# Performance work log

Hardware: AMD Instinct MI355X
Metric: run time of the kernel (lower is better)

## Reference

```python
import jax, jax.numpy as jnp
import numpy as np

B, T, D, H, NB = 4, 2048, 128, 4, 2
DK = D // H
LN_EPS = 1e-3  # keras LayerNormalization default epsilon


def _pos_encoding(maxlen, d):
    # faithful to TransformerNet.get_position_encoding (flat pos-major layout)
    pe = np.array([pos / np.power(10000, 2 * i / d) for pos in range(maxlen) for i in range(d)])
    pe[::2] = np.sin(pe[::2])
    pe[1::2] = np.cos(pe[1::2])
    return jnp.asarray(pe.reshape(maxlen, d), dtype=jnp.float32)


def _ln(x, g, b):
    mu = jnp.mean(x, axis=-1, keepdims=True)
    var = jnp.mean(jnp.square(x - mu), axis=-1, keepdims=True)
    return g * (x - mu) / jnp.sqrt(var + LN_EPS) + b


def setup_inputs() -> dict:
    key = jax.random.key(0)
    ks = jax.random.split(key, 14)
    s = 1.0 / np.sqrt(D)
    w = lambda k, shape: (jax.random.normal(k, shape, jnp.float32) * s)
    return {
        'inputs': jax.random.normal(ks[0], (B, T, D), jnp.float32),
        'Wq': w(ks[1], (NB, D, D)), 'bq': jnp.zeros((NB, D), jnp.float32),
        'Wk': w(ks[2], (NB, D, D)), 'bk': jnp.zeros((NB, D), jnp.float32),
        'Wv': w(ks[3], (NB, D, D)), 'bv': jnp.zeros((NB, D), jnp.float32),
        'Wo': w(ks[4], (NB, D, D)), 'bo': jnp.zeros((NB, D), jnp.float32),
        'W1': w(ks[5], (NB, D, D)), 'b1': jnp.zeros((NB, D), jnp.float32),
        'W2': w(ks[6], (NB, D, D)), 'b2': jnp.zeros((NB, D), jnp.float32),
        'ln_g': jnp.ones((2 * NB, D), jnp.float32),
        'ln_b': jnp.zeros((2 * NB, D), jnp.float32),
    }


def reference(inputs, Wq, bq, Wk, bk, Wv, bv, Wo, bo, W1, b1, W2, b2, ln_g, ln_b):
    h = inputs + _pos_encoding(T, D)[None]  # [B,T,D]
    scale = 1.0 / jnp.sqrt(jnp.float32(DK))
    for i in range(NB):
        # pre-attention LayerNorm
        h = _ln(h, ln_g[2 * i], ln_b[2 * i])
        q = (h @ Wq[i] + bq[i]).reshape(B, T, H, DK)
        k = (h @ Wk[i] + bk[i]).reshape(B, T, H, DK)
        v = (h @ Wv[i] + bv[i]).reshape(B, T, H, DK)
        scores = jnp.einsum('bqhd,bkhd->bhqk', q, k) * scale
        p = jax.nn.softmax(scores, axis=-1)
        # mask is None in TransformerNet.call, but the renormalize step remains
        attn = p / (jnp.sum(p, axis=-1, keepdims=True) + 1e-8)
        ctx = jnp.einsum('bhqk,bkhd->bqhd', attn, v).reshape(B, T, D)
        h = ctx @ Wo[i] + bo[i]  # no residual around attention (as in source)
        # pre-FFN LayerNorm
        h = _ln(h, ln_g[2 * i + 1], ln_b[2 * i + 1])
        # FeedForward with internal residual
        h = h + (jnp.maximum(h @ W1[i] + b1[i], 0.0) @ W2[i] + b2[i])
    # final norm reuses norm_layers[-1] == norm_layers[2*NB-1] (source quirk)
    return _ln(h, ln_g[-1], ln_b[-1])
```

## Files before the change

### kernel.cpp

```cpp
#include <hip/hip_runtime.h>
#include <hip/hip_bf16.h>

typedef __bf16 bf16x8 __attribute__((ext_vector_type(8)));
typedef __bf16 bf16x4 __attribute__((ext_vector_type(4)));
typedef float f32x4 __attribute__((ext_vector_type(4)));
typedef float f32x16 __attribute__((ext_vector_type(16)));
typedef unsigned int u32x4v __attribute__((ext_vector_type(4)));

#define D_ 128
#define T_ 2048
#define B_ 4
#define H_ 4
#define NB_ 2


__global__ __launch_bounds__(256) void prep_weights(
    const float* __restrict__ Wq, const float* __restrict__ Wk,
    const float* __restrict__ Wv, const float* __restrict__ Wo,
    const float* __restrict__ W1, const float* __restrict__ W2,
    __bf16* __restrict__ wp)
{
  int tid = blockIdx.x * 256 + threadIdx.x;
  int e    = tid & 7;
  int lane = (tid >> 3) & 63;
  int ks   = (tid >> 9) & 3;
  int nt   = (tid >> 11) & 7;
  int i    = (tid >> 14) & (NB_ - 1);
  int j    = tid >> 15;
  int k = ks * 32 + (lane >> 4) * 8 + e;
  int n = nt * 16 + (lane & 15);
  const float* srcs[6] = {Wq, Wk, Wv, Wo, W1, W2};
  wp[tid] = (__bf16)srcs[j][i * 16384 + k * 128 + n];
}

__global__ __launch_bounds__(256) void posadd(
    const float* __restrict__ x, __bf16* __restrict__ hp)
{
  int w = threadIdx.x >> 6, lane = threadIdx.x & 63;
  int row = blockIdx.x * 4 + w;
  int t = row & (T_ - 1);
  #pragma unroll
  for (int e = 0; e < 2; e++) {
    int c = lane * 2 + e;
    float arg = (float)t * exp2f(-0.20762050593045952f * (float)c);
    float pe = (c & 1) ? cosf(arg) : sinf(arg);
    float v = x[row * D_ + c] + pe;
    size_t idx = ((size_t)(row >> 4) * 4 + (c >> 5)) * 512 +
                 ((row & 15) + 16 * ((c >> 3) & 3)) * 8 + (c & 7);
    hp[idx] = (__bf16)v;
  }
}

__global__ __launch_bounds__(256) void lnqkv(
    const __bf16* __restrict__ hp, const __bf16* __restrict__ wpq,
    const __bf16* __restrict__ wpk, const __bf16* __restrict__ wpv,
    const float* __restrict__ bq, const float* __restrict__ bk,
    const float* __restrict__ bv, const float* __restrict__ g,
    const float* __restrict__ beta,
    __bf16* __restrict__ qp, __bf16* __restrict__ kp, __bf16* __restrict__ vp)
{
  int w = threadIdx.x >> 6, lane = threadIdx.x & 63;
  int m0 = blockIdx.x * 16;
  int lr = lane & 15, kg = lane >> 4;

  bf16x8 araw[4];
  #pragma unroll
  for (int ks = 0; ks < 4; ks++)
    araw[ks] = *(const bf16x8*)(hp + ((size_t)blockIdx.x * 4 + ks) * 512 + lane * 8);

  float s = 0.f, s2 = 0.f;
  #pragma unroll
  for (int ks = 0; ks < 4; ks++)
    #pragma unroll
    for (int e = 0; e < 8; e++) {
      float x = (float)araw[ks][e];
      s += x; s2 += x * x;
    }
  s += __shfl_xor(s, 16, 64);  s2 += __shfl_xor(s2, 16, 64);
  s += __shfl_xor(s, 32, 64);  s2 += __shfl_xor(s2, 32, 64);
  float mu = s * (1.f / D_);
  float var = s2 * (1.f / D_) - mu * mu;
  float rstd = rsqrtf(var + 1e-3f);

  bf16x8 af[4];
  #pragma unroll
  for (int ks = 0; ks < 4; ks++) {
    int c0 = ks * 32 + kg * 8;
    float4 g0 = *(const float4*)(g + c0), g1 = *(const float4*)(g + c0 + 4);
    float4 q0 = *(const float4*)(beta + c0), q1 = *(const float4*)(beta + c0 + 4);
    const float* gp[2] = {&g0.x, &g1.x};
    const float* bp[2] = {&q0.x, &q1.x};
    #pragma unroll
    for (int e = 0; e < 8; e++)
      af[ks][e] = (__bf16)(((float)araw[ks][e] - mu) * rstd * gp[e >> 2][e & 3] + bp[e >> 2][e & 3]);
  }

  #pragma unroll
  for (int i = 0; i < 2; i++) {
    int nt = w * 2 + i;
    const __bf16* wq = wpq + (size_t)(nt * 4) * 512 + lane * 8;
    const __bf16* wk = wpk + (size_t)(nt * 4) * 512 + lane * 8;
    const __bf16* wv = wpv + (size_t)(nt * 4) * 512 + lane * 8;
    f32x4 aq = {0, 0, 0, 0}, ak = {0, 0, 0, 0}, av = {0, 0, 0, 0};
    #pragma unroll
    for (int ks = 0; ks < 4; ks++) {
      aq = __builtin_amdgcn_mfma_f32_16x16x32_bf16(af[ks], *(const bf16x8*)(wq + ks * 512), aq, 0, 0, 0);
      ak = __builtin_amdgcn_mfma_f32_16x16x32_bf16(af[ks], *(const bf16x8*)(wk + ks * 512), ak, 0, 0, 0);
      av = __builtin_amdgcn_mfma_f32_16x16x32_bf16(af[ks], *(const bf16x8*)(wv + ks * 512), av, 0, 0, 0);
    }
    int col = nt * 16 + lr;
    float bqc = bq[col], bkc = bk[col], bvc = bv[col];
    int dk = i * 16 + lr;
    int hi8 = (lr >> 3) & 1;
    #pragma unroll
    for (int r = 0; r < 4; r++) {
      int row = m0 + kg * 4 + r;
      int bb = row >> 11, tt = row & (T_ - 1);
      size_t qidx = ((((size_t)(bb * 64 + (tt >> 5)) * 4 + w) * 2 + i) * 512) +
                    ((tt & 31) + 32 * hi8) * 8 + (lr & 7);
      qp[qidx] = (__bf16)(aq[r] + bqc);
      size_t kidx = ((((size_t)(bb * 4 + w) * 64 + (tt >> 5)) * 2 + i) * 512) +
                    ((tt & 31) + 32 * hi8) * 8 + (lr & 7);
      kp[kidx] = (__bf16)(ak[r] + bkc);
      size_t vidx = ((((size_t)(bb * 4 + w) * 64 + (tt >> 5)) * 2 + ((tt >> 4) & 1)) * 512) +
                    (dk + 32 * ((tt >> 3) & 1)) * 8 + (tt & 7);
      vp[vidx] = (__bf16)(av[r] + bvc);
    }
  }
}

__global__ __launch_bounds__(512) void attn8(
    const __bf16* __restrict__ qp, const __bf16* __restrict__ kp,
    const __bf16* __restrict__ vp, __bf16* __restrict__ cp)
{
  __shared__ float mbuf[7][64][17];

  int w = threadIdx.x >> 6, lane = threadIdx.x & 63;
  int bh = blockIdx.x & 15, qt = blockIdx.x >> 4;
  int b = bh >> 2, h = bh & 3;
  int lq = lane & 31, hi = lane >> 5;

  const float qscale = 0.17677669529663687f * 1.4426950408889634f;
  const __bf16* qbase = qp + (((size_t)(b * 64 + qt) * 4 + h) * 2) * 512 + lane * 8;
  bf16x8 qraw0 = *(const bf16x8*)(qbase);
  bf16x8 qraw1 = *(const bf16x8*)(qbase + 512);
  bf16x8 qf0, qf1;
  #pragma unroll
  for (int e = 0; e < 8; e++) {
    qf0[e] = (__bf16)((float)qraw0[e] * qscale);
    qf1[e] = (__bf16)((float)qraw1[e] * qscale);
  }

  const __bf16* kbase = kp + ((size_t)(b * 4 + h) * 64) * 1024 + lane * 8;
  const __bf16* vbase = vp + ((size_t)(b * 4 + h) * 64) * 1024 + lane * 8;

  f32x16 acc;
  #pragma unroll
  for (int r = 0; r < 16; r++) acc[r] = 0.f;
  float l = 0.f;

  int kt = w * 8;
  bf16x8 kf0 = *(const bf16x8*)(kbase + (size_t)kt * 1024);
  bf16x8 kf1 = *(const bf16x8*)(kbase + (size_t)kt * 1024 + 512);
  bf16x8 vf0 = *(const bf16x8*)(vbase + (size_t)kt * 1024);
  bf16x8 vf1 = *(const bf16x8*)(vbase + (size_t)kt * 1024 + 512);

  for (int it = 0; it < 8; it++) {
    __builtin_amdgcn_s_setprio(1);
    f32x16 s;
    #pragma unroll
    for (int r = 0; r < 16; r++) s[r] = -24.f;
    s = __builtin_amdgcn_mfma_f32_32x32x16_bf16(kf0, qf0, s, 0, 0, 0);
    s = __builtin_amdgcn_mfma_f32_32x32x16_bf16(kf1, qf1, s, 0, 0, 0);
    __builtin_amdgcn_s_setprio(0);

    bf16x8 kn0, kn1, vn0, vn1;
    if (it < 7) {
      size_t nb = (size_t)(kt + 1) * 1024;
      kn0 = *(const bf16x8*)(kbase + nb);
      kn1 = *(const bf16x8*)(kbase + nb + 512);
      vn0 = *(const bf16x8*)(vbase + nb);
      vn1 = *(const bf16x8*)(vbase + nb + 512);
    }

    unsigned int aw[8];
    #pragma unroll
    for (int g = 0; g < 4; g++) {
      float p0 = __builtin_amdgcn_exp2f(s[g * 4 + 0]);
      float p1 = __builtin_amdgcn_exp2f(s[g * 4 + 1]);
      float p2 = __builtin_amdgcn_exp2f(s[g * 4 + 2]);
      float p3 = __builtin_amdgcn_exp2f(s[g * 4 + 3]);
      l += (p0 + p1) + (p2 + p3);
      unsigned int u01, u23;
      asm("v_cvt_pk_bf16_f32 %0, %1, %2" : "=v"(u01) : "v"(p0), "v"(p1));
      asm("v_cvt_pk_bf16_f32 %0, %1, %2" : "=v"(u23) : "v"(p2), "v"(p3));
      aw[g * 2] = u01; aw[g * 2 + 1] = u23;
    }
    unsigned int a0 = aw[0], a2 = aw[2];
    asm volatile("v_permlane32_swap_b32 %0, %1" : "+v"(a0), "+v"(a2));
    unsigned int a1 = aw[1], a3 = aw[3];
    asm volatile("v_permlane32_swap_b32 %0, %1" : "+v"(a1), "+v"(a3));
    bf16x8 pw0 = __builtin_bit_cast(bf16x8, (u32x4v){a0, a1, a2, a3});
    unsigned int a4 = aw[4], a6 = aw[6];
    asm volatile("v_permlane32_swap_b32 %0, %1" : "+v"(a4), "+v"(a6));
    unsigned int a5 = aw[5], a7 = aw[7];
    asm volatile("v_permlane32_swap_b32 %0, %1" : "+v"(a5), "+v"(a7));
    bf16x8 pw1 = __builtin_bit_cast(bf16x8, (u32x4v){a4, a5, a6, a7});

    __builtin_amdgcn_s_setprio(1);
    acc = __builtin_amdgcn_mfma_f32_32x32x16_bf16(vf0, pw0, acc, 0, 0, 0);
    acc = __builtin_amdgcn_mfma_f32_32x32x16_bf16(vf1, pw1, acc, 0, 0, 0);
    __builtin_amdgcn_s_setprio(0);

    kf0 = kn0; kf1 = kn1; vf0 = vn0; vf1 = vn1;
    kt += 1;
  }

  l += __shfl_xor(l, 32, 64);

  if (w > 0) {
    float* mb = &mbuf[w - 1][lane][0];
    #pragma unroll
    for (int r = 0; r < 16; r++) mb[r] = acc[r];
    mb[16] = l;
  }
  __syncthreads();
  if (w == 0) {
    #pragma unroll
    for (int w2_ = 0; w2_ < 7; w2_++) {
      const float* mb = &mbuf[w2_][lane][0];
      #pragma unroll
      for (int r = 0; r < 16; r++) acc[r] += mb[r];
      l += mb[16];
    }
    float inv = 1.f / l;
    __bf16* cbase = cp + ((size_t)(b * 128 + qt * 2 + (lq >> 4)) * 4 + h) * 512 + 4 * hi;
    #pragma unroll
    for (int g = 0; g < 4; g++) {
      bf16x4 o;
      #pragma unroll
      for (int j = 0; j < 4; j++) o[j] = (__bf16)(acc[g * 4 + j] * inv);
      *(bf16x4*)(cbase + ((lq & 15) + 16 * g) * 8) = o;
    }
  }
}

__global__ __launch_bounds__(256) void wo_ffn_qkv(
    const __bf16* __restrict__ cp, const __bf16* __restrict__ wpo,
    const float* __restrict__ bo, const float* __restrict__ g1,
    const float* __restrict__ bt1, const __bf16* __restrict__ wp1,
    const float* __restrict__ b1, const __bf16* __restrict__ wp2,
    const float* __restrict__ b2,
    const float* __restrict__ gq, const float* __restrict__ btq,
    const __bf16* __restrict__ wpq, const __bf16* __restrict__ wpk,
    const __bf16* __restrict__ wpv,
    const float* __restrict__ bq, const float* __restrict__ bk,
    const float* __restrict__ bv,
    __bf16* __restrict__ qp, __bf16* __restrict__ kp, __bf16* __restrict__ vp)
{
  __shared__ __attribute__((aligned(16))) __bf16 tb0[16][128];
  __shared__ __attribute__((aligned(16))) __bf16 tb1[16][128];
  __shared__ float2 statb[16][4];

  int w = threadIdx.x >> 6, lane = threadIdx.x & 63;
  int m0 = blockIdx.x * 16;
  int lr = lane & 15, kg = lane >> 4;
  int swz = (lr & 7) << 3;

  bf16x8 af[4];
  #pragma unroll
  for (int ks = 0; ks < 4; ks++)
    af[ks] = *(const bf16x8*)(cp + ((size_t)blockIdx.x * 4 + ks) * 512 + lane * 8);

  f32x4 acc[2] = {{0, 0, 0, 0}, {0, 0, 0, 0}};
  #pragma unroll
  for (int i = 0; i < 2; i++) {
    const __bf16* wrow = wpo + (size_t)((w * 2 + i) * 4) * 512 + lane * 8;
    #pragma unroll
    for (int ks = 0; ks < 4; ks++)
      acc[i] = __builtin_amdgcn_mfma_f32_16x16x32_bf16(af[ks], *(const bf16x8*)(wrow + ks * 512), acc[i], 0, 0, 0);
  }

  float xv[2][4];
  float s[4] = {0, 0, 0, 0}, s2[4] = {0, 0, 0, 0};
  #pragma unroll
  for (int i = 0; i < 2; i++) {
    float bcol = bo[(w * 2 + i) * 16 + lr];
    #pragma unroll
    for (int r = 0; r < 4; r++) {
      float y = acc[i][r] + bcol;
      xv[i][r] = y; s[r] += y; s2[r] += y * y;
    }
  }
  #pragma unroll
  for (int r = 0; r < 4; r++)
    for (int mk = 1; mk < 16; mk <<= 1) {
      s[r] += __shfl_xor(s[r], mk, 64);
      s2[r] += __shfl_xor(s2[r], mk, 64);
    }
  if (lr == 0) {
    #pragma unroll
    for (int r = 0; r < 4; r++) statb[kg * 4 + r][w] = make_float2(s[r], s2[r]);
  }
  __syncthreads();
  float mu_[4], rstd_[4];
  #pragma unroll
  for (int r = 0; r < 4; r++) {
    int row = kg * 4 + r;
    float ss = 0.f, ss2 = 0.f;
    #pragma unroll
    for (int w2 = 0; w2 < 4; w2++) {
      float2 t = statb[row][w2];
      ss += t.x; ss2 += t.y;
    }
    mu_[r] = ss * (1.f / D_);
    float var = ss2 * (1.f / D_) - mu_[r] * mu_[r];
    rstd_[r] = rsqrtf(var + 1e-3f);
  }
  float hres[2][4];
  #pragma unroll
  for (int i = 0; i < 2; i++) {
    int col = (w * 2 + i) * 16 + lr;
    float gc = g1[col], bc = bt1[col];
    #pragma unroll
    for (int r = 0; r < 4; r++) {
      float y = (xv[i][r] - mu_[r]) * rstd_[r] * gc + bc;
      hres[i][r] = y;
      int row = kg * 4 + r;
      tb0[row][col ^ ((row & 7) << 3)] = (__bf16)y;
    }
  }
  __syncthreads();

  bf16x8 a2[4];
  #pragma unroll
  for (int ks = 0; ks < 4; ks++)
    a2[ks] = *(const bf16x8*)(&tb0[lr][(ks * 32 + kg * 8) ^ swz]);
  f32x4 acc2[2] = {{0, 0, 0, 0}, {0, 0, 0, 0}};
  #pragma unroll
  for (int i = 0; i < 2; i++) {
    const __bf16* wrow = wp1 + (size_t)((w * 2 + i) * 4) * 512 + lane * 8;
    #pragma unroll
    for (int ks = 0; ks < 4; ks++)
      acc2[i] = __builtin_amdgcn_mfma_f32_16x16x32_bf16(a2[ks], *(const bf16x8*)(wrow + ks * 512), acc2[i], 0, 0, 0);
  }
  #pragma unroll
  for (int i = 0; i < 2; i++) {
    float bcol = b1[(w * 2 + i) * 16 + lr];
    int col = (w * 2 + i) * 16 + lr;
    #pragma unroll
    for (int r = 0; r < 4; r++) {
      int row = kg * 4 + r;
      tb1[row][col ^ ((row & 7) << 3)] = (__bf16)fmaxf(acc2[i][r] + bcol, 0.f);
    }
  }
  __syncthreads();

  bf16x8 a3[4];
  #pragma unroll
  for (int ks = 0; ks < 4; ks++)
    a3[ks] = *(const bf16x8*)(&tb1[lr][(ks * 32 + kg * 8) ^ swz]);
  f32x4 acc3[2] = {{0, 0, 0, 0}, {0, 0, 0, 0}};
  #pragma unroll
  for (int i = 0; i < 2; i++) {
    const __bf16* wrow = wp2 + (size_t)((w * 2 + i) * 4) * 512 + lane * 8;
    #pragma unroll
    for (int ks = 0; ks < 4; ks++)
      acc3[i] = __builtin_amdgcn_mfma_f32_16x16x32_bf16(a3[ks], *(const bf16x8*)(wrow + ks * 512), acc3[i], 0, 0, 0);
  }

  #pragma unroll
  for (int i = 0; i < 2; i++) {
    int col = (w * 2 + i) * 16 + lr;
    float bcol = b2[col];
    #pragma unroll
    for (int r = 0; r < 4; r++) {
      int row = kg * 4 + r;
      tb0[row][col ^ ((row & 7) << 3)] = (__bf16)(acc3[i][r] + bcol + hres[i][r]);
    }
  }
  __syncthreads();

  bf16x8 araw[4];
  #pragma unroll
  for (int ks = 0; ks < 4; ks++)
    araw[ks] = *(const bf16x8*)(&tb0[lr][(ks * 32 + kg * 8) ^ swz]);
  float t = 0.f, t2 = 0.f;
  #pragma unroll
  for (int ks = 0; ks < 4; ks++)
    #pragma unroll
    for (int e = 0; e < 8; e++) {
      float x = (float)araw[ks][e];
      t += x; t2 += x * x;
    }
  t += __shfl_xor(t, 16, 64);  t2 += __shfl_xor(t2, 16, 64);
  t += __shfl_xor(t, 32, 64);  t2 += __shfl_xor(t2, 32, 64);
  float mu = t * (1.f / D_);
  float var = t2 * (1.f / D_) - mu * mu;
  float rstd = rsqrtf(var + 1e-3f);

  bf16x8 af2[4];
  #pragma unroll
  for (int ks = 0; ks < 4; ks++) {
    int c0 = ks * 32 + kg * 8;
    float4 g0 = *(const float4*)(gq + c0), g1v = *(const float4*)(gq + c0 + 4);
    float4 q0 = *(const float4*)(btq + c0), q1 = *(const float4*)(btq + c0 + 4);
    const float* gp[2] = {&g0.x, &g1v.x};
    const float* bp[2] = {&q0.x, &q1.x};
    #pragma unroll
    for (int e = 0; e < 8; e++)
      af2[ks][e] = (__bf16)(((float)araw[ks][e] - mu) * rstd * gp[e >> 2][e & 3] + bp[e >> 2][e & 3]);
  }

  #pragma unroll
  for (int i = 0; i < 2; i++) {
    int nt = w * 2 + i;
    const __bf16* wq = wpq + (size_t)(nt * 4) * 512 + lane * 8;
    const __bf16* wk = wpk + (size_t)(nt * 4) * 512 + lane * 8;
    const __bf16* wv = wpv + (size_t)(nt * 4) * 512 + lane * 8;
    f32x4 aq = {0, 0, 0, 0}, ak = {0, 0, 0, 0}, av = {0, 0, 0, 0};
    #pragma unroll
    for (int ks = 0; ks < 4; ks++) {
      aq = __builtin_amdgcn_mfma_f32_16x16x32_bf16(af2[ks], *(const bf16x8*)(wq + ks * 512), aq, 0, 0, 0);
      ak = __builtin_amdgcn_mfma_f32_16x16x32_bf16(af2[ks], *(const bf16x8*)(wk + ks * 512), ak, 0, 0, 0);
      av = __builtin_amdgcn_mfma_f32_16x16x32_bf16(af2[ks], *(const bf16x8*)(wv + ks * 512), av, 0, 0, 0);
    }
    int col = nt * 16 + lr;
    float bqc = bq[col], bkc = bk[col], bvc = bv[col];
    int dk = i * 16 + lr;
    int hi8 = (lr >> 3) & 1;
    #pragma unroll
    for (int r = 0; r < 4; r++) {
      int row = m0 + kg * 4 + r;
      int bb = row >> 11, tt = row & (T_ - 1);
      size_t qidx = ((((size_t)(bb * 64 + (tt >> 5)) * 4 + w) * 2 + i) * 512) +
                    ((tt & 31) + 32 * hi8) * 8 + (lr & 7);
      qp[qidx] = (__bf16)(aq[r] + bqc);
      size_t kidx = ((((size_t)(bb * 4 + w) * 64 + (tt >> 5)) * 2 + i) * 512) +
                    ((tt & 31) + 32 * hi8) * 8 + (lr & 7);
      kp[kidx] = (__bf16)(ak[r] + bkc);
      size_t vidx = ((((size_t)(bb * 4 + w) * 64 + (tt >> 5)) * 2 + ((tt >> 4) & 1)) * 512) +
                    (dk + 32 * ((tt >> 3) & 1)) * 8 + (tt & 7);
      vp[vidx] = (__bf16)(av[r] + bvc);
    }
  }
}

__global__ __launch_bounds__(256) void wo_ffn_last(
    const __bf16* __restrict__ cp, const __bf16* __restrict__ wpo,
    const float* __restrict__ bo, const float* __restrict__ g1,
    const float* __restrict__ bt1, const __bf16* __restrict__ wp1,
    const float* __restrict__ b1, const __bf16* __restrict__ wp2,
    const float* __restrict__ b2, const float* __restrict__ g2,
    const float* __restrict__ bt2, float* __restrict__ outf)
{
  __shared__ __attribute__((aligned(16))) __bf16 tb0[16][128];
  __shared__ __attribute__((aligned(16))) __bf16 tb1[16][128];
  __shared__ float2 statb[16][4];

  int w = threadIdx.x >> 6, lane = threadIdx.x & 63;
  int m0 = blockIdx.x * 16;
  int lr = lane & 15, kg = lane >> 4;
  int swz = (lr & 7) << 3;

  bf16x8 af[4];
  #pragma unroll
  for (int ks = 0; ks < 4; ks++)
    af[ks] = *(const bf16x8*)(cp + ((size_t)blockIdx.x * 4 + ks) * 512 + lane * 8);

  f32x4 acc[2] = {{0, 0, 0, 0}, {0, 0, 0, 0}};
  #pragma unroll
  for (int i = 0; i < 2; i++) {
    const __bf16* wrow = wpo + (size_t)((w * 2 + i) * 4) * 512 + lane * 8;
    #pragma unroll
    for (int ks = 0; ks < 4; ks++)
      acc[i] = __builtin_amdgcn_mfma_f32_16x16x32_bf16(af[ks], *(const bf16x8*)(wrow + ks * 512), acc[i], 0, 0, 0);
  }

  float xv[2][4];
  float s[4] = {0, 0, 0, 0}, s2[4] = {0, 0, 0, 0};
  #pragma unroll
  for (int i = 0; i < 2; i++) {
    float bcol = bo[(w * 2 + i) * 16 + lr];
    #pragma unroll
    for (int r = 0; r < 4; r++) {
      float y = acc[i][r] + bcol;
      xv[i][r] = y; s[r] += y; s2[r] += y * y;
    }
  }
  #pragma unroll
  for (int r = 0; r < 4; r++)
    for (int mk = 1; mk < 16; mk <<= 1) {
      s[r] += __shfl_xor(s[r], mk, 64);
      s2[r] += __shfl_xor(s2[r], mk, 64);
    }
  if (lr == 0) {
    #pragma unroll
    for (int r = 0; r < 4; r++) statb[kg * 4 + r][w] = make_float2(s[r], s2[r]);
  }
  __syncthreads();
  float mu_[4], rstd_[4];
  #pragma unroll
  for (int r = 0; r < 4; r++) {
    int row = kg * 4 + r;
    float ss = 0.f, ss2 = 0.f;
    #pragma unroll
    for (int w2 = 0; w2 < 4; w2++) {
      float2 t = statb[row][w2];
      ss += t.x; ss2 += t.y;
    }
    mu_[r] = ss * (1.f / D_);
    float var = ss2 * (1.f / D_) - mu_[r] * mu_[r];
    rstd_[r] = rsqrtf(var + 1e-3f);
  }
  float hres[2][4];
  #pragma unroll
  for (int i = 0; i < 2; i++) {
    int col = (w * 2 + i) * 16 + lr;
    float gc = g1[col], bc = bt1[col];
    #pragma unroll
    for (int r = 0; r < 4; r++) {
      float y = (xv[i][r] - mu_[r]) * rstd_[r] * gc + bc;
      hres[i][r] = y;
      int row = kg * 4 + r;
      tb0[row][col ^ ((row & 7) << 3)] = (__bf16)y;
    }
  }
  __syncthreads();

  bf16x8 a2[4];
  #pragma unroll
  for (int ks = 0; ks < 4; ks++)
    a2[ks] = *(const bf16x8*)(&tb0[lr][(ks * 32 + kg * 8) ^ swz]);
  f32x4 acc2[2] = {{0, 0, 0, 0}, {0, 0, 0, 0}};
  #pragma unroll
  for (int i = 0; i < 2; i++) {
    const __bf16* wrow = wp1 + (size_t)((w * 2 + i) * 4) * 512 + lane * 8;
    #pragma unroll
    for (int ks = 0; ks < 4; ks++)
      acc2[i] = __builtin_amdgcn_mfma_f32_16x16x32_bf16(a2[ks], *(const bf16x8*)(wrow + ks * 512), acc2[i], 0, 0, 0);
  }
  #pragma unroll
  for (int i = 0; i < 2; i++) {
    float bcol = b1[(w * 2 + i) * 16 + lr];
    int col = (w * 2 + i) * 16 + lr;
    #pragma unroll
    for (int r = 0; r < 4; r++) {
      int row = kg * 4 + r;
      tb1[row][col ^ ((row & 7) << 3)] = (__bf16)fmaxf(acc2[i][r] + bcol, 0.f);
    }
  }
  __syncthreads();

  bf16x8 a3[4];
  #pragma unroll
  for (int ks = 0; ks < 4; ks++)
    a3[ks] = *(const bf16x8*)(&tb1[lr][(ks * 32 + kg * 8) ^ swz]);
  f32x4 acc3[2] = {{0, 0, 0, 0}, {0, 0, 0, 0}};
  #pragma unroll
  for (int i = 0; i < 2; i++) {
    const __bf16* wrow = wp2 + (size_t)((w * 2 + i) * 4) * 512 + lane * 8;
    #pragma unroll
    for (int ks = 0; ks < 4; ks++)
      acc3[i] = __builtin_amdgcn_mfma_f32_16x16x32_bf16(a3[ks], *(const bf16x8*)(wrow + ks * 512), acc3[i], 0, 0, 0);
  }

  float yv[2][4];
  float t[4] = {0, 0, 0, 0}, t2[4] = {0, 0, 0, 0};
  #pragma unroll
  for (int i = 0; i < 2; i++) {
    float bcol = b2[(w * 2 + i) * 16 + lr];
    #pragma unroll
    for (int r = 0; r < 4; r++) {
      float y = acc3[i][r] + bcol + hres[i][r];
      yv[i][r] = y; t[r] += y; t2[r] += y * y;
    }
  }
  #pragma unroll
  for (int r = 0; r < 4; r++)
    for (int mk = 1; mk < 16; mk <<= 1) {
      t[r] += __shfl_xor(t[r], mk, 64);
      t2[r] += __shfl_xor(t2[r], mk, 64);
    }
  __syncthreads();
  if (lr == 0) {
    #pragma unroll
    for (int r = 0; r < 4; r++) statb[kg * 4 + r][w] = make_float2(t[r], t2[r]);
  }
  __syncthreads();
  #pragma unroll
  for (int r = 0; r < 4; r++) {
    int row = kg * 4 + r;
    float ss = 0.f, ss2 = 0.f;
    #pragma unroll
    for (int w2 = 0; w2 < 4; w2++) {
      float2 tt = statb[row][w2];
      ss += tt.x; ss2 += tt.y;
    }
    float mu = ss * (1.f / D_);
    float var = ss2 * (1.f / D_) - mu * mu;
    float rstd = rsqrtf(var + 1e-3f);
    #pragma unroll
    for (int i = 0; i < 2; i++) {
      int col = (w * 2 + i) * 16 + lr;
      outf[(size_t)(m0 + row) * D_ + col] =
          (yv[i][r] - mu) * rstd * g2[col] + bt2[col];
    }
  }
}

extern "C" void kernel_launch(void* const* d_in, const int* in_sizes, int n_in,
                              void* d_out, int out_size, void* d_ws, size_t ws_size,
                              hipStream_t stream)
{
  const float* inputs = (const float*)d_in[0];
  const float* Wq = (const float*)d_in[1];
  const float* bq = (const float*)d_in[2];
  const float* Wk = (const float*)d_in[3];
  const float* bk = (const float*)d_in[4];
  const float* Wv = (const float*)d_in[5];
  const float* bv = (const float*)d_in[6];
  const float* Wo = (const float*)d_in[7];
  const float* bo = (const float*)d_in[8];
  const float* W1 = (const float*)d_in[9];
  const float* b1 = (const float*)d_in[10];
  const float* W2 = (const float*)d_in[11];
  const float* b2 = (const float*)d_in[12];
  const float* ln_g = (const float*)d_in[13];
  const float* ln_b = (const float*)d_in[14];
  float* out = (float*)d_out;

  char* ws = (char*)d_ws;
  size_t off = 0;
  auto alloc = [&](size_t bytes) {
    void* p = ws + off;
    off = (off + bytes + 255) & ~(size_t)255;
    return p;
  };
  const size_t ACT = (size_t)8192 * 128 * sizeof(__bf16);
  __bf16* wp = (__bf16*)alloc((size_t)6 * NB_ * 16384 * sizeof(__bf16));
  __bf16* hp = (__bf16*)alloc(ACT);
  __bf16* qp = (__bf16*)alloc(ACT);
  __bf16* kp = (__bf16*)alloc(ACT);
  __bf16* vp = (__bf16*)alloc(ACT);
  __bf16* cb = (__bf16*)alloc(ACT);

  prep_weights<<<768, 256, 0, stream>>>(Wq, Wk, Wv, Wo, W1, W2, wp);
  posadd<<<2048, 256, 0, stream>>>(inputs, hp);

  const __bf16* wpq0 = wp + (size_t)(0 * NB_ + 0) * 16384;
  const __bf16* wpk0 = wp + (size_t)(1 * NB_ + 0) * 16384;
  const __bf16* wpv0 = wp + (size_t)(2 * NB_ + 0) * 16384;
  const __bf16* wpo0 = wp + (size_t)(3 * NB_ + 0) * 16384;
  const __bf16* wp10 = wp + (size_t)(4 * NB_ + 0) * 16384;
  const __bf16* wp20 = wp + (size_t)(5 * NB_ + 0) * 16384;
  const __bf16* wpq1 = wp + (size_t)(0 * NB_ + 1) * 16384;
  const __bf16* wpk1 = wp + (size_t)(1 * NB_ + 1) * 16384;
  const __bf16* wpv1 = wp + (size_t)(2 * NB_ + 1) * 16384;
  const __bf16* wpo1 = wp + (size_t)(3 * NB_ + 1) * 16384;
  const __bf16* wp11 = wp + (size_t)(4 * NB_ + 1) * 16384;
  const __bf16* wp21 = wp + (size_t)(5 * NB_ + 1) * 16384;

  lnqkv<<<512, 256, 0, stream>>>(hp, wpq0, wpk0, wpv0, bq, bk, bv,
                                 ln_g, ln_b, qp, kp, vp);
  attn8<<<1024, 512, 0, stream>>>(qp, kp, vp, cb);
  wo_ffn_qkv<<<512, 256, 0, stream>>>(cb, wpo0, bo,
                                      ln_g + 128, ln_b + 128, wp10, b1, wp20, b2,
                                      ln_g + 2 * 128, ln_b + 2 * 128,
                                      wpq1, wpk1, wpv1,
                                      bq + 128, bk + 128, bv + 128,
                                      qp, kp, vp);
  attn8<<<1024, 512, 0, stream>>>(qp, kp, vp, cb);
  wo_ffn_last<<<512, 256, 0, stream>>>(cb, wpo1, bo + 128,
                                       ln_g + 3 * 128, ln_b + 3 * 128,
                                       wp11, b1 + 128, wp21, b2 + 128,
                                       ln_g + 3 * 128, ln_b + 3 * 128, out);
}
```

Before: 148.3 us.

## Fuse positional encoding into LN-QKV and process two query tiles per attention block

The posadd kernel is removed and the positional encoding is computed inside the first LN+QKV kernel directly from fp32 inputs, which drops one launch and the bf16 intermediate round trip. The attention kernel now handles two 32-row query tiles per block and reuses each loaded K/V fragment for both. This halves the grid and the total K/V traffic. The cost is more registers and a larger shared reduction buffer, which may reduce occupancy, and sin/cos is now computed redundantly across the four waves.

```diff
diff --git a/kernel.cpp b/kernel.cpp
--- a/kernel.cpp
+++ b/kernel.cpp
@@ -33,26 +33,8 @@
   wp[tid] = (__bf16)srcs[j][i * 16384 + k * 128 + n];
 }
 
-__global__ __launch_bounds__(256) void posadd(
-    const float* __restrict__ x, __bf16* __restrict__ hp)
-{
-  int w = threadIdx.x >> 6, lane = threadIdx.x & 63;
-  int row = blockIdx.x * 4 + w;
-  int t = row & (T_ - 1);
-  #pragma unroll
-  for (int e = 0; e < 2; e++) {
-    int c = lane * 2 + e;
-    float arg = (float)t * exp2f(-0.20762050593045952f * (float)c);
-    float pe = (c & 1) ? cosf(arg) : sinf(arg);
-    float v = x[row * D_ + c] + pe;
-    size_t idx = ((size_t)(row >> 4) * 4 + (c >> 5)) * 512 +
-                 ((row & 15) + 16 * ((c >> 3) & 3)) * 8 + (c & 7);
-    hp[idx] = (__bf16)v;
-  }
-}
-
-__global__ __launch_bounds__(256) void lnqkv(
-    const __bf16* __restrict__ hp, const __bf16* __restrict__ wpq,
+__global__ __launch_bounds__(256) void posln_qkv(
+    const float* __restrict__ x, const __bf16* __restrict__ wpq,
     const __bf16* __restrict__ wpk, const __bf16* __restrict__ wpv,
     const float* __restrict__ bq, const float* __restrict__ bk,
     const float* __restrict__ bv, const float* __restrict__ g,
@@ -62,20 +44,26 @@
   int w = threadIdx.x >> 6, lane = threadIdx.x & 63;
   int m0 = blockIdx.x * 16;
   int lr = lane & 15, kg = lane >> 4;
-
-  bf16x8 araw[4];
-  #pragma unroll
-  for (int ks = 0; ks < 4; ks++)
-    araw[ks] = *(const bf16x8*)(hp + ((size_t)blockIdx.x * 4 + ks) * 512 + lane * 8);
-
+  int row = m0 + lr;
+  int t = row & (T_ - 1);
+
+  float araw[4][8];
   float s = 0.f, s2 = 0.f;
   #pragma unroll
-  for (int ks = 0; ks < 4; ks++)
+  for (int ks = 0; ks < 4; ks++) {
+    const float* xr = x + (size_t)row * D_ + ks * 32 + kg * 8;
+    float4 x0 = *(const float4*)(xr);
+    float4 x1 = *(const float4*)(xr + 4);
+    const float* xv[2] = {&x0.x, &x1.x};
     #pragma unroll
     for (int e = 0; e < 8; e++) {
-      float x = (float)araw[ks][e];
-      s += x; s2 += x * x;
-    }
+      int c = ks * 32 + kg * 8 + e;
+      float arg = (float)t * exp2f(-0.20762050593045952f * (float)c);
+      float pe = (c & 1) ? cosf(arg) : sinf(arg);
+      float v = xv[e >> 2][e & 3] + pe;
+      araw[ks][e] = v; s += v; s2 += v * v;
+    }
+  }
   s += __shfl_xor(s, 16, 64);  s2 += __shfl_xor(s2, 16, 64);
   s += __shfl_xor(s, 32, 64);  s2 += __shfl_xor(s2, 32, 64);
   float mu = s * (1.f / D_);
@@ -92,7 +80,7 @@
     const float* bp[2] = {&q0.x, &q1.x};
     #pragma unroll
     for (int e = 0; e < 8; e++)
-      af[ks][e] = (__bf16)(((float)araw[ks][e] - mu) * rstd * gp[e >> 2][e & 3] + bp[e >> 2][e & 3]);
+      af[ks][e] = (__bf16)((araw[ks][e] - mu) * rstd * gp[e >> 2][e & 3] + bp[e >> 2][e & 3]);
   }
 
   #pragma unroll
@@ -114,8 +102,8 @@
     int hi8 = (lr >> 3) & 1;
     #pragma unroll
     for (int r = 0; r < 4; r++) {
-      int row = m0 + kg * 4 + r;
-      int bb = row >> 11, tt = row & (T_ - 1);
+      int rw = m0 + kg * 4 + r;
+      int bb = rw >> 11, tt = rw & (T_ - 1);
       size_t qidx = ((((size_t)(bb * 64 + (tt >> 5)) * 4 + w) * 2 + i) * 512) +
                     ((tt & 31) + 32 * hi8) * 8 + (lr & 7);
       qp[qidx] = (__bf16)(aq[r] + bqc);
@@ -129,35 +117,43 @@
   }
 }
 
-__global__ __launch_bounds__(512) void attn8(
+__global__ __launch_bounds__(512) void attn9(
     const __bf16* __restrict__ qp, const __bf16* __restrict__ kp,
     const __bf16* __restrict__ vp, __bf16* __restrict__ cp)
 {
-  __shared__ float mbuf[7][64][17];
+  __shared__ float mbuf[7][64][35];
 
   int w = threadIdx.x >> 6, lane = threadIdx.x & 63;
-  int bh = blockIdx.x & 15, qt = blockIdx.x >> 4;
+  int bh = blockIdx.x & 15, qtp = blockIdx.x >> 4;
   int b = bh >> 2, h = bh & 3;
   int lq = lane & 31, hi = lane >> 5;
+  int qtA = qtp * 2, qtB = qtp * 2 + 1;
 
   const float qscale = 0.17677669529663687f * 1.4426950408889634f;
-  const __bf16* qbase = qp + (((size_t)(b * 64 + qt) * 4 + h) * 2) * 512 + lane * 8;
-  bf16x8 qraw0 = *(const bf16x8*)(qbase);
-  bf16x8 qraw1 = *(const bf16x8*)(qbase + 512);
-  bf16x8 qf0, qf1;
-  #pragma unroll
-  for (int e = 0; e < 8; e++) {
-    qf0[e] = (__bf16)((float)qraw0[e] * qscale);
-    qf1[e] = (__bf16)((float)qraw1[e] * qscale);
+  const __bf16* qbaseA = qp + (((size_t)(b * 64 + qtA) * 4 + h) * 2) * 512 + lane * 8;
+  const __bf16* qbaseB = qp + (((size_t)(b * 64 + qtB) * 4 + h) * 2) * 512 + lane * 8;
+  bf16x8 qA0, qA1, qB0, qB1;
+  {
+    bf16x8 ra0 = *(const bf16x8*)(qbaseA);
+    bf16x8 ra1 = *(const bf16x8*)(qbaseA + 512);
+    bf16x8 rb0 = *(const bf16x8*)(qbaseB);
+    bf16x8 rb1 = *(const bf16x8*)(qbaseB + 512);
+    #pragma unroll
+    for (int e = 0; e < 8; e++) {
+      qA0[e] = (__bf16)((float)ra0[e] * qscale);
+      qA1[e] = (__bf16)((float)ra1[e] * qscale);
+      qB0[e] = (__bf16)((float)rb0[e] * qscale);
+      qB1[e] = (__bf16)((float)rb1[e] * qscale);
+    }
   }
 
   const __bf16* kbase = kp + ((size_t)(b * 4 + h) * 64) * 1024 + lane * 8;
   const __bf16* vbase = vp + ((size_t)(b * 4 + h) * 64) * 1024 + lane * 8;
 
-  f32x16 acc;
-  #pragma unroll
-  for (int r = 0; r < 16; r++) acc[r] = 0.f;
-  float l = 0.f;
+  f32x16 accA, accB;
+  #pragma unroll
+  for (int r = 0; r < 16; r++) { accA[r] = 0.f; accB[r] = 0.f; }
+  float lA = 0.f, lB = 0.f;
 
   int kt = w * 8;
   bf16x8 kf0 = *(const bf16x8*)(kbase + (size_t)kt * 1024);
@@ -166,14 +162,6 @@
   bf16x8 vf1 = *(const bf16x8*)(vbase + (size_t)kt * 1024 + 512);
 
   for (int it = 0; it < 8; it++) {
-    __builtin_amdgcn_s_setprio(1);
-    f32x16 s;
-    #pragma unroll
-    for (int r = 0; r < 16; r++) s[r] = -24.f;
-    s = __builtin_amdgcn_mfma_f32_32x32x16_bf16(kf0, qf0, s, 0, 0, 0);
-    s = __builtin_amdgcn_mfma_f32_32x32x16_bf16(kf1, qf1, s, 0, 0, 0);
-    __builtin_amdgcn_s_setprio(0);
-
     bf16x8 kn0, kn1, vn0, vn1;
     if (it < 7) {
       size_t nb = (size_t)(kt + 1) * 1024;
@@ -183,46 +171,92 @@
       vn1 = *(const bf16x8*)(vbase + nb + 512);
     }
 
-    unsigned int aw[8];
-    #pragma unroll
-    for (int g = 0; g < 4; g++) {
-      float p0 = __builtin_amdgcn_exp2f(s[g * 4 + 0]);
-      float p1 = __builtin_amdgcn_exp2f(s[g * 4 + 1]);
-      float p2 = __builtin_amdgcn_exp2f(s[g * 4 + 2]);
-      float p3 = __builtin_amdgcn_exp2f(s[g * 4 + 3]);
-      l += (p0 + p1) + (p2 + p3);
-      unsigned int u01, u23;
-      asm("v_cvt_pk_bf16_f32 %0, %1, %2" : "=v"(u01) : "v"(p0), "v"(p1));
-      asm("v_cvt_pk_bf16_f32 %0, %1, %2" : "=v"(u23) : "v"(p2), "v"(p3));
-      aw[g * 2] = u01; aw[g * 2 + 1] = u23;
-    }
-    unsigned int a0 = aw[0], a2 = aw[2];
-    asm volatile("v_permlane32_swap_b32 %0, %1" : "+v"(a0), "+v"(a2));
-    unsigned int a1 = aw[1], a3 = aw[3];
-    asm volatile("v_permlane32_swap_b32 %0, %1" : "+v"(a1), "+v"(a3));
-    bf16x8 pw0 = __builtin_bit_cast(bf16x8, (u32x4v){a0, a1, a2, a3});
-    unsigned int a4 = aw[4], a6 = aw[6];
-    asm volatile("v_permlane32_swap_b32 %0, %1" : "+v"(a4), "+v"(a6));
-    unsigned int a5 = aw[5], a7 = aw[7];
-    asm volatile("v_permlane32_swap_b32 %0, %1" : "+v"(a5), "+v"(a7));
-    bf16x8 pw1 = __builtin_bit_cast(bf16x8, (u32x4v){a4, a5, a6, a7});
+    bf16x8 pwA0, pwA1;
+    {
+      __builtin_amdgcn_s_setprio(1);
+      f32x16 s;
+      #pragma unroll
+      for (int r = 0; r < 16; r++) s[r] = -24.f;
+      s = __builtin_amdgcn_mfma_f32_32x32x16_bf16(kf0, qA0, s, 0, 0, 0);
+      s = __builtin_amdgcn_mfma_f32_32x32x16_bf16(kf1, qA1, s, 0, 0, 0);
+      __builtin_amdgcn_s_setprio(0);
+      unsigned int aw[8];
+      #pragma unroll
+      for (int g = 0; g < 4; g++) {
+        float p0 = __builtin_amdgcn_exp2f(s[g * 4 + 0]);
+        float p1 = __builtin_amdgcn_exp2f(s[g * 4 + 1]);
+        float p2 = __builtin_amdgcn_exp2f(s[g * 4 + 2]);
+        float p3 = __builtin_amdgcn_exp2f(s[g * 4 + 3]);
+        lA += (p0 + p1) + (p2 + p3);
+        unsigned int u01, u23;
+        asm("v_cvt_pk_bf16_f32 %0, %1, %2" : "=v"(u01) : "v"(p0), "v"(p1));
+        asm("v_cvt_pk_bf16_f32 %0, %1, %2" : "=v"(u23) : "v"(p2), "v"(p3));
+        aw[g * 2] = u01; aw[g * 2 + 1] = u23;
+      }
+      unsigned int a0 = aw[0], a2 = aw[2];
+      asm volatile("v_permlane32_swap_b32 %0, %1" : "+v"(a0), "+v"(a2));
+      unsigned int a1 = aw[1], a3 = aw[3];
+      asm volatile("v_permlane32_swap_b32 %0, %1" : "+v"(a1), "+v"(a3));
+      pwA0 = __builtin_bit_cast(bf16x8, (u32x4v){a0, a1, a2, a3});
+      unsigned int a4 = aw[4], a6 = aw[6];
+      asm volatile("v_permlane32_swap_b32 %0, %1" : "+v"(a4), "+v"(a6));
+      unsigned int a5 = aw[5], a7 = aw[7];
+      asm volatile("v_permlane32_swap_b32 %0, %1" : "+v"(a5), "+v"(a7));
+      pwA1 = __builtin_bit_cast(bf16x8, (u32x4v){a4, a5, a6, a7});
+    }
+    bf16x8 pwB0, pwB1;
+    {
+      __builtin_amdgcn_s_setprio(1);
+      f32x16 s;
+      #pragma unroll
+      for (int r = 0; r < 16; r++) s[r] = -24.f;
+      s = __builtin_amdgcn_mfma_f32_32x32x16_bf16(kf0, qB0, s, 0, 0, 0);
+      s = __builtin_amdgcn_mfma_f32_32x32x16_bf16(kf1, qB1, s, 0, 0, 0);
+      __builtin_amdgcn_s_setprio(0);
+      unsigned int aw[8];
+      #pragma unroll
+      for (int g = 0; g < 4; g++) {
+        float p0 = __builtin_amdgcn_exp2f(s[g * 4 + 0]);
+        float p1 = __builtin_amdgcn_exp2f(s[g * 4 + 1]);
+        float p2 = __builtin_amdgcn_exp2f(s[g * 4 + 2]);
+        float p3 = __builtin_amdgcn_exp2f(s[g * 4 + 3]);
+        lB += (p0 + p1) + (p2 + p3);
+        unsigned int u01, u23;
+        asm("v_cvt_pk_bf16_f32 %0, %1, %2" : "=v"(u01) : "v"(p0), "v"(p1));
+        asm("v_cvt_pk_bf16_f32 %0, %1, %2" : "=v"(u23) : "v"(p2), "v"(p3));
+        aw[g * 2] = u01; aw[g * 2 + 1] = u23;
+      }
+      unsigned int a0 = aw[0], a2 = aw[2];
+      asm volatile("v_permlane32_swap_b32 %0, %1" : "+v"(a0), "+v"(a2));
+      unsigned int a1 = aw[1], a3 = aw[3];
+      asm volatile("v_permlane32_swap_b32 %0, %1" : "+v"(a1), "+v"(a3));
+      pwB0 = __builtin_bit_cast(bf16x8, (u32x4v){a0, a1, a2, a3});
+      unsigned int a4 = aw[4], a6 = aw[6];
+      asm volatile("v_permlane32_swap_b32 %0, %1" : "+v"(a4), "+v"(a6));
+      unsigned int a5 = aw[5], a7 = aw[7];
+      asm volatile("v_permlane32_swap_b32 %0, %1" : "+v"(a5), "+v"(a7));
+      pwB1 = __builtin_bit_cast(bf16x8, (u32x4v){a4, a5, a6, a7});
+    }
 
     __builtin_amdgcn_s_setprio(1);
-    acc = __builtin_amdgcn_mfma_f32_32x32x16_bf16(vf0, pw0, acc, 0, 0, 0);
-    acc = __builtin_amdgcn_mfma_f32_32x32x16_bf16(vf1, pw1, acc, 0, 0, 0);
+    accA = __builtin_amdgcn_mfma_f32_32x32x16_bf16(vf0, pwA0, accA, 0, 0, 0);
+    accA = __builtin_amdgcn_mfma_f32_32x32x16_bf16(vf1, pwA1, accA, 0, 0, 0);
+    accB = __builtin_amdgcn_mfma_f32_32x32x16_bf16(vf0, pwB0, accB, 0, 0, 0);
+    accB = __builtin_amdgcn_mfma_f32_32x32x16_bf16(vf1, pwB1, accB, 0, 0, 0);
     __builtin_amdgcn_s_setprio(0);
 
     kf0 = kn0; kf1 = kn1; vf0 = vn0; vf1 = vn1;
     kt += 1;
   }
 
-  l += __shfl_xor(l, 32, 64);
+  lA += __shfl_xor(lA, 32, 64);
+  lB += __shfl_xor(lB, 32, 64);
 
   if (w > 0) {
     float* mb = &mbuf[w - 1][lane][0];
     #pragma unroll
-    for (int r = 0; r < 16; r++) mb[r] = acc[r];
-    mb[16] = l;
+    for (int r = 0; r < 16; r++) { mb[r] = accA[r]; mb[16 + r] = accB[r]; }
+    mb[32] = lA; mb[33] = lB;
   }
   __syncthreads();
   if (w == 0) {
@@ -230,17 +264,22 @@
     for (int w2_ = 0; w2_ < 7; w2_++) {
       const float* mb = &mbuf[w2_][lane][0];
       #pragma unroll
-      for (int r = 0; r < 16; r++) acc[r] += mb[r];
-      l += mb[16];
-    }
-    float inv = 1.f / l;
-    __bf16* cbase = cp + ((size_t)(b * 128 + qt * 2 + (lq >> 4)) * 4 + h) * 512 + 4 * hi;
+      for (int r = 0; r < 16; r++) { accA[r] += mb[r]; accB[r] += mb[16 + r]; }
+      lA += mb[32]; lB += mb[33];
+    }
+    float invA = 1.f / lA, invB = 1.f / lB;
+    __bf16* cbA = cp + ((size_t)(b * 128 + qtA * 2 + (lq >> 4)) * 4 + h) * 512 + 4 * hi;
+    __bf16* cbB = cp + ((size_t)(b * 128 + qtB * 2 + (lq >> 4)) * 4 + h) * 512 + 4 * hi;
     #pragma unroll
     for (int g = 0; g < 4; g++) {
-      bf16x4 o;
+      bf16x4 oA, oB;
       #pragma unroll
-      for (int j = 0; j < 4; j++) o[j] = (__bf16)(acc[g * 4 + j] * inv);
-      *(bf16x4*)(cbase + ((lq & 15) + 16 * g) * 8) = o;
+      for (int j = 0; j < 4; j++) {
+        oA[j] = (__bf16)(accA[g * 4 + j] * invA);
+        oB[j] = (__bf16)(accB[g * 4 + j] * invB);
+      }
+      *(bf16x4*)(cbA + ((lq & 15) + 16 * g) * 8) = oA;
+      *(bf16x4*)(cbB + ((lq & 15) + 16 * g) * 8) = oB;
     }
   }
 }
@@ -639,14 +678,12 @@
   };
   const size_t ACT = (size_t)8192 * 128 * sizeof(__bf16);
   __bf16* wp = (__bf16*)alloc((size_t)6 * NB_ * 16384 * sizeof(__bf16));
-  __bf16* hp = (__bf16*)alloc(ACT);
   __bf16* qp = (__bf16*)alloc(ACT);
   __bf16* kp = (__bf16*)alloc(ACT);
   __bf16* vp = (__bf16*)alloc(ACT);
   __bf16* cb = (__bf16*)alloc(ACT);
 
   prep_weights<<<768, 256, 0, stream>>>(Wq, Wk, Wv, Wo, W1, W2, wp);
-  posadd<<<2048, 256, 0, stream>>>(inputs, hp);
 
   const __bf16* wpq0 = wp + (size_t)(0 * NB_ + 0) * 16384;
   const __bf16* wpk0 = wp + (size_t)(1 * NB_ + 0) * 16384;
@@ -661,16 +698,16 @@
   const __bf16* wp11 = wp + (size_t)(4 * NB_ + 1) * 16384;
   const __bf16* wp21 = wp + (size_t)(5 * NB_ + 1) * 16384;
 
-  lnqkv<<<512, 256, 0, stream>>>(hp, wpq0, wpk0, wpv0, bq, bk, bv,
-                                 ln_g, ln_b, qp, kp, vp);
-  attn8<<<1024, 512, 0, stream>>>(qp, kp, vp, cb);
+  posln_qkv<<<512, 256, 0, stream>>>(inputs, wpq0, wpk0, wpv0, bq, bk, bv,
+                                     ln_g, ln_b, qp, kp, vp);
+  attn9<<<512, 512, 0, stream>>>(qp, kp, vp, cb);
   wo_ffn_qkv<<<512, 256, 0, stream>>>(cb, wpo0, bo,
                                       ln_g + 128, ln_b + 128, wp10, b1, wp20, b2,
                                       ln_g + 2 * 128, ln_b + 2 * 128,
                                       wpq1, wpk1, wpv1,
                                       bq + 128, bk + 128, bv + 128,
                                       qp, kp, vp);
-  attn8<<<1024, 512, 0, stream>>>(qp, kp, vp, cb);
+  attn9<<<512, 512, 0, stream>>>(qp, kp, vp, cb);
   wo_ffn_last<<<512, 256, 0, stream>>>(cb, wpo1, bo + 128,
                                        ln_g + 3 * 128, ln_b + 3 * 128,
                                        wp11, b1 + 128, wp21, b2 + 128,
```

Measured after the change: 149.2 us. Within noise of the previous version (+0.6%).
